# Optimization experiments

Hardware: AMD Instinct MI355X
Metric: run time of the kernel (lower is better)

## Reference

```python
import jax, jax.numpy as jnp
import numpy as np

EPS = 1e-5

def _conv3x3(x, w, b):
    # NCHW, OIHW, 3x3 stride 1 pad 1
    y = jax.lax.conv_general_dilated(x, w, window_strides=(1, 1),
                                     padding=((1, 1), (1, 1)),
                                     dimension_numbers=('NCHW', 'OIHW', 'NCHW'))
    return y + b[None, :, None, None]

def _pool_upsample(x, k):
    # adaptive avg pool to (H/k, W/k) then nearest block-upsample back
    B, C, H, W = x.shape
    p = x.reshape(B, C, H // k, k, W // k, k).mean(axis=(3, 5))
    return jnp.repeat(jnp.repeat(p, k, axis=2), k, axis=3)

def setup_inputs() -> dict:
    key = jax.random.key(0)
    ks = jax.random.split(key, 12)
    B, C, H, W = 32, 8, 300, 300
    d = {
        'x': jax.random.normal(ks[0], (B, C, H, W), jnp.float32),
        'w5': jax.random.normal(ks[1], (8, 16, 3, 3), jnp.float32) * 0.1,
        'b5': jnp.zeros((8,), jnp.float32),
        'w10': jax.random.normal(ks[2], (8, 16, 3, 3), jnp.float32) * 0.1,
        'b10': jnp.zeros((8,), jnp.float32),
        'w15': jax.random.normal(ks[3], (8, 16, 3, 3), jnp.float32) * 0.1,
        'b15': jnp.zeros((8,), jnp.float32),
        'gw': jax.random.normal(ks[4], (8, 24, 3, 3), jnp.float32) * 0.1,
        'gb': jnp.zeros((8,), jnp.float32),
        'mw': jax.random.normal(ks[5], (8, 24, 3, 3), jnp.float32) * 0.1,
        'mb': jnp.zeros((8,), jnp.float32),
        'gamma': jnp.ones((8,), jnp.float32),
        'beta': jnp.zeros((8,), jnp.float32),
    }
    return d

def reference(x, w5, b5, w10, b10, w15, b15, gw, gb, mw, mb, gamma, beta):
    up5 = _pool_upsample(x, 5)    # [B,8,300,300]
    up10 = _pool_upsample(x, 10)
    up15 = _pool_upsample(x, 15)
    c5 = _conv3x3(jnp.concatenate([x, up5], axis=1), w5, b5)
    c10 = _conv3x3(jnp.concatenate([x, up10], axis=1), w10, b10)
    c15 = _conv3x3(jnp.concatenate([x, up15], axis=1), w15, b15)
    g_in = jnp.concatenate([c5, c10, c15], axis=1)  # [B,24,H,W]
    # gated conv, activation=None: conv(g_in) * sigmoid(mask_conv(g_in))
    y = _conv3x3(g_in, gw, gb) * jax.nn.sigmoid(_conv3x3(g_in, mw, mb))
    # batch norm (training-mode batch stats, biased var, as torch default)
    mean = y.mean(axis=(0, 2, 3), keepdims=True)
    var = ((y - mean) ** 2).mean(axis=(0, 2, 3), keepdims=True)
    y = (y - mean) * jax.lax.rsqrt(var + EPS)
    return y * gamma[None, :, None, None] + beta[None, :, None, None]
```

## Files before the change

### kernel.cpp

```cpp
#include <hip/hip_runtime.h>
#include <math.h>

typedef __bf16 bfrag __attribute__((ext_vector_type(8)));
typedef __bf16 bf16x4 __attribute__((ext_vector_type(4)));
typedef __bf16 bf16x8 __attribute__((ext_vector_type(8)));
typedef float f32x4 __attribute__((ext_vector_type(4)));

#define BN 32
#define HH 300
#define WW 300
#define HW 90000
#define NPX (BN * HW)

#define GX 10
#define GY 19
#define CPX 612
#define XPX 720
#define CWSTRIDE 4896

#define P5I_BYTE_OFF   0
#define P10I_BYTE_OFF  1843200
#define P15I_BYTE_OFF  2304000
#define CWB_BYTE_OFF   2508800
#define GWB_BYTE_OFF   2524160
#define STAT_BYTE_OFF  2531328
#define SS_BYTE_OFF    2539520
#define XBF_BYTE_OFF   2539584
#define XBF_END        (XBF_BYTE_OFF + (size_t)NPX * 16)

__device__ __forceinline__ short f2bf(float f) {
    union { float f; unsigned u; } v;
    v.f = f;
    unsigned r = v.u + 0x7FFF + ((v.u >> 16) & 1);
    return (short)(r >> 16);
}

__device__ __forceinline__ float bf2f(unsigned short s) {
    union { unsigned u; float f; } v;
    v.u = ((unsigned)s) << 16;
    return v.f;
}

__device__ __forceinline__ void setup_body(int gid, int gstride,
                                           const float* __restrict__ w5,
                                           const float* __restrict__ w10,
                                           const float* __restrict__ w15,
                                           const float* __restrict__ gw,
                                           const float* __restrict__ mw,
                                           short* __restrict__ cBg,
                                           short* __restrict__ gBg,
                                           double* __restrict__ stats) {
    for (int idx = gid; idx < 7680; idx += gstride) {
        int s = idx / 2560, rem = idx % 2560;
        int n = rem / 160, r2 = rem % 160;
        int tap = r2 / 16, ci = r2 % 16;
        float v = 0.f;
        if (n < 8 && tap < 9) {
            const float* W = (s == 0) ? w5 : ((s == 1) ? w10 : w15);
            v = W[(n * 16 + ci) * 9 + tap];
        }
        cBg[idx] = f2bf(v);
    }
    for (int idx = gid; idx < 3584; idx += gstride) {
        int n = idx / 224, r2 = idx % 224;
        int blk = r2 / 8, cj = r2 % 8;
        float v = 0.f;
        if (blk < 27) {
            int tap = blk / 3, ci24 = (blk % 3) * 8 + cj;
            if (n < 8) v = gw[(n * 24 + ci24) * 9 + tap];
            else       v = mw[((n - 8) * 24 + ci24) * 9 + tap];
        }
        gBg[idx] = f2bf(v);
    }
    for (int idx = gid; idx < 16 * 64; idx += gstride) stats[idx] = 0.0;
}

__global__ void k_setup(const float* __restrict__ w5, const float* __restrict__ w10,
                        const float* __restrict__ w15, const float* __restrict__ gw,
                        const float* __restrict__ mw, short* __restrict__ cBg,
                        short* __restrict__ gBg, double* __restrict__ stats) {
    setup_body(threadIdx.x, 256, w5, w10, w15, gw, mw, cBg, gBg, stats);
}

__global__ __launch_bounds__(256) void k_xbf(const float* __restrict__ x,
                                             unsigned short* __restrict__ xbf,
                                             const float* __restrict__ w5,
                                             const float* __restrict__ w10,
                                             const float* __restrict__ w15,
                                             const float* __restrict__ gw,
                                             const float* __restrict__ mw,
                                             short* __restrict__ cBg,
                                             short* __restrict__ gBg,
                                             double* __restrict__ stats) {
    const int b = blockIdx.y;
    const int px = blockIdx.x * 256 + threadIdx.x;
    if (px < HW) {
        const float* xp = x + (size_t)b * 8 * HW + px;
        bf16x8 pk;
#pragma unroll
        for (int ch = 0; ch < 8; ch++) pk[ch] = (__bf16)xp[(size_t)ch * HW];
        *(bf16x8*)&xbf[((size_t)b * HW + px) * 8] = pk;
    }
    if (blockIdx.y == 0 && blockIdx.x < 16) {
        int gid = blockIdx.x * 256 + threadIdx.x;
        setup_body(gid, 4096, w5, w10, w15, gw, mw, cBg, gBg, stats);
    }
}

__global__ void k_pool5(const float* __restrict__ x, unsigned short* __restrict__ p5i) {
    int id = blockIdx.x * 256 + threadIdx.x;
    int bc = id / 3600, cell = id % 3600;
    int b = bc >> 3, c = bc & 7;
    int pi = cell / 60, pj = cell % 60;
    const float* rp = x + (size_t)bc * HW + pi * 5 * WW + pj * 5;
    float s = 0.f;
#pragma unroll
    for (int u = 0; u < 5; u++)
#pragma unroll
        for (int v = 0; v < 5; v++) s += rp[u * WW + v];
    p5i[((size_t)b * 3600 + cell) * 8 + c] = (unsigned short)f2bf(s * 0.04f);
}

__global__ __launch_bounds__(256) void k_pool5b(const unsigned short* __restrict__ xbf,
                                                unsigned short* __restrict__ p5i) {
    int id = blockIdx.x * 256 + threadIdx.x;
    int b = id / 3600, cell = id % 3600;
    int pi = cell / 60, pj = cell % 60;
    const unsigned short* base = xbf + ((size_t)b * HW + pi * 5 * WW + pj * 5) * 8;
    float s[8] = {0.f, 0.f, 0.f, 0.f, 0.f, 0.f, 0.f, 0.f};
#pragma unroll
    for (int u = 0; u < 5; u++)
#pragma unroll
        for (int v = 0; v < 5; v++) {
            bf16x8 vv = *(const bf16x8*)&base[(u * WW + v) * 8];
#pragma unroll
            for (int ch = 0; ch < 8; ch++) s[ch] += (float)vv[ch];
        }
    bf16x8 pk;
#pragma unroll
    for (int ch = 0; ch < 8; ch++) pk[ch] = (__bf16)(s[ch] * 0.04f);
    *(bf16x8*)&p5i[((size_t)b * 3600 + cell) * 8] = pk;
}

__global__ void k_poolD(const unsigned short* __restrict__ p5i,
                        unsigned short* __restrict__ p10i,
                        unsigned short* __restrict__ p15i) {
    int id = blockIdx.x * 256 + threadIdx.x;
    if (id < 230400) {
        int bc = id / 900, cell = id % 900;
        int b = bc >> 3, c = bc & 7;
        int pi = cell / 30, pj = cell % 30;
        const unsigned short* base = p5i + ((size_t)b * 3600) * 8 + c;
        float s = bf2f(base[((2 * pi) * 60 + 2 * pj) * 8]) +
                  bf2f(base[((2 * pi) * 60 + 2 * pj + 1) * 8]) +
                  bf2f(base[((2 * pi + 1) * 60 + 2 * pj) * 8]) +
                  bf2f(base[((2 * pi + 1) * 60 + 2 * pj + 1) * 8]);
        p10i[((size_t)b * 900 + cell) * 8 + c] = (unsigned short)f2bf(s * 0.25f);
    } else if (id < 332800) {
        int id2 = id - 230400;
        int bc = id2 / 400, cell = id2 % 400;
        int b = bc >> 3, c = bc & 7;
        int pi = cell / 20, pj = cell % 20;
        const unsigned short* base = p5i + ((size_t)b * 3600) * 8 + c;
        float s = 0.f;
#pragma unroll
        for (int u = 0; u < 3; u++)
#pragma unroll
            for (int v = 0; v < 3; v++)
                s += bf2f(base[((3 * pi + u) * 60 + 3 * pj + v) * 8]);
        p15i[((size_t)b * 400 + cell) * 8 + c] = (unsigned short)f2bf(s * (1.f / 9.f));
    }
}

template <int K, int PW>
__device__ __forceinline__ void up_load(const unsigned short* __restrict__ pooled,
                                        int b, int r0, int c0, int t, uint4* v) {
#pragma unroll
    for (int it = 0; it < 3; it++) {
        int idx = t + 256 * it;
        uint4 val = {0u, 0u, 0u, 0u};
        if (idx < XPX) {
            int i = idx / 36, j = idx - i * 36;
            int ra = r0 - 2 + i, ca = c0 - 2 + j;
            if (ra >= 0 && ra < HH && ca >= 0 && ca < WW) {
                int pi = (int)((unsigned)ra / K);
                int pj = (int)((unsigned)ca / K);
                val = *(const uint4*)&pooled[((size_t)b * (PW * PW) + pi * PW + pj) * 8];
            }
        }
        v[it] = val;
    }
}

__device__ __forceinline__ void up_store(short* xuU, int t, const uint4* v) {
#pragma unroll
    for (int it = 0; it < 3; it++) {
        int idx = t + 256 * it;
        if (idx < XPX) *(uint4*)&xuU[idx * 8] = v[it];
    }
}

__device__ __forceinline__ void c_phase(const short* xuX, const short* xuU,
                                        short* cwP,
                                        const unsigned short* __restrict__ cBs,
                                        const float* __restrict__ bias,
                                        int r0, int c0, int lane, int wid, bool edge) {
    const int n = lane & 15, quad = lane >> 4;
    const int qh = quad >> 1, ql = quad & 1;
    const short* xbase = ql ? xuU : xuX;
    bfrag wfr[5];
    int dpoff[5];
#pragma unroll
    for (int km = 0; km < 5; km++) {
        int tapw = km * 2 + qh;
        int tapa = (tapw > 8) ? 8 : tapw;
        wfr[km] = *(const bfrag*)&cBs[(n * 10 + tapw) * 16 + ql * 8];
        dpoff[km] = ((tapa / 3) * 36 + tapa % 3) * 8;
    }
    float bO[4];
#pragma unroll
    for (int r = 0; r < 4; r++) bO[r] = bias[(quad & 1) * 4 + r];

    for (int g = wid; g < 39; g += 4) {
        int px = g * 16 + n;
        if (px > 611) px = 611;
        int rp = (int)((unsigned)px / 34u);
        int cp = px - rp * 34;
        int pb = (rp * 36 + cp) * 8;
        f32x4 acc = {0.f, 0.f, 0.f, 0.f};
#pragma unroll
        for (int km = 0; km < 5; km++)
            acc = __builtin_amdgcn_mfma_f32_16x16x32_bf16(
                wfr[km], *(const bfrag*)&xbase[pb + dpoff[km]], acc, 0, 0, 0);
        if (quad < 2) {
            bf16x4 pk;
#pragma unroll
            for (int r = 0; r < 4; r++) pk[r] = (__bf16)(acc[r] + bO[r]);
            if (edge) {
                int ra = r0 - 1 + rp, ca = c0 - 1 + cp;
                if (ra < 0 || ra >= HH || ca < 0 || ca >= WW) {
#pragma unroll
                    for (int r = 0; r < 4; r++) pk[r] = (__bf16)0.f;
                }
            }
            *(bf16x4*)&cwP[px * 8 + quad * 4] = pk;
        }
    }
}

template <bool XBF>
__global__ __launch_bounds__(256, 3) void k_fused(
    const float* __restrict__ x, const unsigned short* __restrict__ xbf,
    const unsigned short* __restrict__ p5i, const unsigned short* __restrict__ p10i,
    const unsigned short* __restrict__ p15i,
    const unsigned short* __restrict__ cBg, const unsigned short* __restrict__ gBg,
    const float* __restrict__ b5, const float* __restrict__ b10, const float* __restrict__ b15,
    const float* __restrict__ gb, const float* __restrict__ mb,
    float* __restrict__ out, double* __restrict__ stats) {
    __shared__ __align__(16) short xuX[XPX * 8];
    __shared__ __align__(16) short xuU[XPX * 8];
    __shared__ __align__(16) short cwS[3 * CWSTRIDE];

    const int b = blockIdx.z;
    const int r0 = blockIdx.y * 16, c0 = blockIdx.x * 32;
    const int t = threadIdx.x, lane = t & 63, wid = t >> 6;
    const bool edge = (blockIdx.x == 0) | (blockIdx.x == GX - 1) |
                      (blockIdx.y == 0) | (blockIdx.y == GY - 1);

    uint4 upv[3];
    up_load<5, 60>(p5i, b, r0, c0, t, upv);

    if constexpr (XBF) {
#pragma unroll
        for (int it = 0; it < 3; it++) {
            int idx = t + 256 * it;
            if (idx < XPX) {
                int i = idx / 36, j = idx - i * 36;
                int ra = r0 - 2 + i, ca = c0 - 2 + j;
                uint4 v = {0u, 0u, 0u, 0u};
                if (ra >= 0 && ra < HH && ca >= 0 && ca < WW)
                    v = *(const uint4*)&xbf[((size_t)b * HW + ra * WW + ca) * 8];
                *(uint4*)&xuX[idx * 8] = v;
            }
        }
    } else {
        for (int idx = t; idx < 1440; idx += 256) {
            int cp = idx / 360, rem = idx % 360;
            int i = rem / 18, jp = rem % 18;
            int j = 2 * jp;
            int ra = r0 - 2 + i, ca = c0 - 2 + j;
            float2 v0 = {0.f, 0.f}, v1 = {0.f, 0.f};
            if (ra >= 0 && ra < HH && ca >= 0 && ca <= WW - 2) {
                size_t base = ((size_t)(b * 8 + 2 * cp) * HH + ra) * WW + ca;
                v0 = *(const float2*)&x[base];
                v1 = *(const float2*)&x[base + HW];
            }
            unsigned pA = (unsigned short)f2bf(v0.x) | ((unsigned)(unsigned short)f2bf(v1.x) << 16);
            unsigned pB = (unsigned short)f2bf(v0.y) | ((unsigned)(unsigned short)f2bf(v1.y) << 16);
            int px = i * 36 + j;
            *(unsigned*)&xuX[px * 8 + 2 * cp] = pA;
            *(unsigned*)&xuX[(px + 1) * 8 + 2 * cp] = pB;
        }
    }
    up_store(xuU, t, upv);
    __syncthreads();

    c_phase(xuX, xuU, cwS, cBg, b5, r0, c0, lane, wid, edge);
    up_load<10, 30>(p10i, b, r0, c0, t, upv);
    __syncthreads();
    up_store(xuU, t, upv);
    __syncthreads();

    c_phase(xuX, xuU, cwS + CWSTRIDE, cBg + 2560, b10, r0, c0, lane, wid, edge);
    up_load<15, 20>(p15i, b, r0, c0, t, upv);
    __syncthreads();
    up_store(xuU, t, upv);
    __syncthreads();

    c_phase(xuX, xuU, cwS + 2 * CWSTRIDE, cBg + 5120, b15, r0, c0, lane, wid, edge);
    __syncthreads();

    const int n = lane & 15, quad = lane >> 4;
    bfrag gfr[7];
    int goff[7];
#pragma unroll
    for (int km = 0; km < 7; km++) {
        int blkw = km * 4 + quad;
        int blka = (blkw > 26) ? 26 : blkw;
        gfr[km] = *(const bfrag*)&gBg[(n * 28 + blkw) * 8];
        int tap = blka / 3, cig = blka - tap * 3;
        goff[km] = cig * CWSTRIDE + ((tap / 3) * 34 + tap % 3) * 8;
    }
    float gO[4], mO[4];
#pragma unroll
    for (int r = 0; r < 4; r++) {
        gO[r] = gb[(quad & 1) * 4 + r];
        mO[r] = mb[(quad & 1) * 4 + r];
    }
    float ls[4] = {0.f, 0.f, 0.f, 0.f}, ls2[4] = {0.f, 0.f, 0.f, 0.f};

    for (int g = wid; g < 32; g += 4) {
        int px = g * 16 + n;
        int rr = px >> 5, cc = px & 31;
        int off0 = (rr * 34 + cc) * 8;
        f32x4 acc = {0.f, 0.f, 0.f, 0.f};
#pragma unroll
        for (int km = 0; km < 7; km++)
            acc = __builtin_amdgcn_mfma_f32_16x16x32_bf16(
                gfr[km], *(const bfrag*)&cwS[off0 + goff[km]], acc, 0, 0, 0);
        int ra = r0 + rr, ca = c0 + cc;
        bool wr = !edge || (ra < HH && ca < WW);
#pragma unroll
        for (int reg = 0; reg < 4; reg++) {
            float val;
            if (quad < 2) val = acc[reg] + gO[reg];
            else          val = __builtin_amdgcn_rcpf(1.f + __expf(-(acc[reg] + mO[reg])));
            float other = __shfl_xor(val, 32);
            if (quad < 2 && wr) {
                float y = val * other;
                int ch = quad * 4 + reg;
                out[(size_t)(b * 8 + ch) * HW + (size_t)ra * WW + ca] = y;
                ls[reg] += y;
                ls2[reg] += y * y;
            }
        }
    }
#pragma unroll
    for (int m = 1; m < 16; m <<= 1) {
#pragma unroll
        for (int r = 0; r < 4; r++) {
            ls[r] += __shfl_xor(ls[r], m);
            ls2[r] += __shfl_xor(ls2[r], m);
        }
    }
    if (n == 0 && quad < 2) {
        int hash = (blockIdx.x + GX * blockIdx.y + GX * GY * blockIdx.z) & 63;
#pragma unroll
        for (int r = 0; r < 4; r++) {
            atomicAdd(&stats[(quad * 4 + r) * 64 + hash], (double)ls[r]);
            atomicAdd(&stats[(8 + quad * 4 + r) * 64 + hash], (double)ls2[r]);
        }
    }
}

__global__ void k_stats(const double* __restrict__ stats, const float* __restrict__ gamma,
                        const float* __restrict__ beta, float* __restrict__ ss) {
    __shared__ double red[16][16];
    int t = threadIdx.x;
    int row = t >> 4, col = t & 15;
    double s = stats[row * 64 + col] + stats[row * 64 + col + 16] +
               stats[row * 64 + col + 32] + stats[row * 64 + col + 48];
    red[row][col] = s;
    __syncthreads();
    if (t < 16) {
        double tot = 0.0;
#pragma unroll
        for (int i = 0; i < 16; i++) tot += red[t][i];
        red[t][0] = tot;
    }
    __syncthreads();
    if (t < 8) {
        double N = (double)NPX;
        double mean = red[t][0] / N;
        double var = red[8 + t][0] / N - mean * mean;
        double scale = (double)gamma[t] / sqrt(var + 1e-5);
        ss[t] = (float)scale;
        ss[8 + t] = (float)((double)beta[t] - mean * scale);
    }
}

__global__ void k_norm(float* __restrict__ out, const float* __restrict__ ss) {
    int i = blockIdx.x * 256 + threadIdx.x;
    if (i < (BN * 8 * HW) / 4) {
        int plane = (i * 4) / HW;
        int ch = plane & 7;
        float sc = ss[ch], sh = ss[8 + ch];
        float4* p = (float4*)out + i;
        float4 v = *p;
        v.x = v.x * sc + sh;
        v.y = v.y * sc + sh;
        v.z = v.z * sc + sh;
        v.w = v.w * sc + sh;
        *p = v;
    }
}

extern "C" void kernel_launch(void* const* d_in, const int* in_sizes, int n_in,
                              void* d_out, int out_size, void* d_ws, size_t ws_size,
                              hipStream_t stream) {
    const float* x = (const float*)d_in[0];
    const float* w5 = (const float*)d_in[1];
    const float* b5 = (const float*)d_in[2];
    const float* w10 = (const float*)d_in[3];
    const float* b10 = (const float*)d_in[4];
    const float* w15 = (const float*)d_in[5];
    const float* b15 = (const float*)d_in[6];
    const float* gw = (const float*)d_in[7];
    const float* gb = (const float*)d_in[8];
    const float* mw = (const float*)d_in[9];
    const float* mb = (const float*)d_in[10];
    const float* gamma = (const float*)d_in[11];
    const float* beta = (const float*)d_in[12];

    float* out = (float*)d_out;
    unsigned short* p5i = (unsigned short*)((char*)d_ws + P5I_BYTE_OFF);
    unsigned short* p10i = (unsigned short*)((char*)d_ws + P10I_BYTE_OFF);
    unsigned short* p15i = (unsigned short*)((char*)d_ws + P15I_BYTE_OFF);
    short* cBg = (short*)((char*)d_ws + CWB_BYTE_OFF);
    short* gBg = (short*)((char*)d_ws + GWB_BYTE_OFF);
    double* stats = (double*)((char*)d_ws + STAT_BYTE_OFF);
    float* ss = (float*)((char*)d_ws + SS_BYTE_OFF);
    unsigned short* xbf = (unsigned short*)((char*)d_ws + XBF_BYTE_OFF);

    const bool use_xbf = (ws_size >= XBF_END);

    dim3 grid(GX, GY, BN);
    if (use_xbf) {
        k_xbf<<<dim3(352, 32), 256, 0, stream>>>(x, xbf, w5, w10, w15, gw, mw,
                                                 cBg, gBg, stats);
        k_pool5b<<<450, 256, 0, stream>>>(xbf, p5i);
        k_poolD<<<1300, 256, 0, stream>>>(p5i, p10i, p15i);
        k_fused<true><<<grid, 256, 0, stream>>>(x, xbf, p5i, p10i, p15i,
                                                (const unsigned short*)cBg, (const unsigned short*)gBg,
                                                b5, b10, b15, gb, mb, out, stats);
    } else {
        k_setup<<<1, 256, 0, stream>>>(w5, w10, w15, gw, mw, cBg, gBg, stats);
        k_pool5<<<3600, 256, 0, stream>>>(x, p5i);
        k_poolD<<<1300, 256, 0, stream>>>(p5i, p10i, p15i);
        k_fused<false><<<grid, 256, 0, stream>>>(x, xbf, p5i, p10i, p15i,
                                                 (const unsigned short*)cBg, (const unsigned short*)gBg,
                                                 b5, b10, b15, gb, mb, out, stats);
    }
    k_stats<<<1, 256, 0, stream>>>(stats, gamma, beta, ss);
    k_norm<<<(BN * 8 * HW / 4 + 255) / 256, 256, 0, stream>>>(out, ss);
}
```

Before: 387.4 us.

## Use padded per-batch bf16 slabs and fuse pooling into one prep kernel

Adds a new path that writes x plus the 5/10/15 pooled maps into zero-padded per-batch bf16 slabs in a single prep kernel, with pool10 and pool15 derived from pool5 in shared memory. The fused conv kernel then gathers MFMA operands straight from global memory through row/column offset lookup tables, with no staging of inputs into LDS, and padding removes the bounds checks. This cuts the number of launches and the separate pooling passes. It needs a larger workspace, and it relies on uncoalesced global gathers hitting in cache.

```diff
diff --git a/kernel.cpp b/kernel.cpp
--- a/kernel.cpp
+++ b/kernel.cpp
@@ -27,6 +27,21 @@
 #define SS_BYTE_OFF    2539520
 #define XBF_BYTE_OFF   2539584
 #define XBF_END        (XBF_BYTE_OFF + (size_t)NPX * 16)
+
+#define XW 302
+#define P5W 62
+#define P10W 32
+#define P15W 22
+#define XOFF5  (XW * XW * 16)
+#define XOFF10 (XOFF5 + P5W * P5W * 16)
+#define XOFF15 (XOFF10 + P10W * P10W * 16)
+#define SLAB   (XOFF15 + P15W * P15W * 16)
+#define CWB2_OFF  0
+#define GWB2_OFF  15360
+#define STAT2_OFF 22528
+#define SS2_OFF   30720
+#define SLAB_OFF  32768
+#define NEW_END   (SLAB_OFF + (size_t)BN * SLAB)
 
 __device__ __forceinline__ short f2bf(float f) {
     union { float f; unsigned u; } v;
@@ -80,6 +95,266 @@
                         const float* __restrict__ mw, short* __restrict__ cBg,
                         short* __restrict__ gBg, double* __restrict__ stats) {
     setup_body(threadIdx.x, 256, w5, w10, w15, gw, mw, cBg, gBg, stats);
+}
+
+__global__ __launch_bounds__(256) void k_prep2(const float* __restrict__ x,
+                                               char* __restrict__ slabs,
+                                               const float* __restrict__ w5,
+                                               const float* __restrict__ w10,
+                                               const float* __restrict__ w15,
+                                               const float* __restrict__ gw,
+                                               const float* __restrict__ mw,
+                                               short* __restrict__ cBg,
+                                               short* __restrict__ gBg,
+                                               double* __restrict__ stats) {
+    __shared__ __align__(16) short p5L[3600 * 8];
+    const int b = blockIdx.y, t = threadIdx.x;
+    char* slab = slabs + (size_t)b * SLAB;
+
+    if (blockIdx.x < 357) {
+        int p = blockIdx.x * 256 + t;
+        if (p < XW * XW) {
+            int pr = p / XW, pc = p - pr * XW;
+            if (pr >= 1 && pr <= 300 && pc >= 1 && pc <= 300) {
+                const float* xp = x + (size_t)b * 8 * HW + (pr - 1) * WW + (pc - 1);
+                bf16x8 pk;
+#pragma unroll
+                for (int ch = 0; ch < 8; ch++) pk[ch] = (__bf16)xp[ch * HW];
+                *(bf16x8*)(slab + (size_t)p * 16) = pk;
+            } else {
+                uint4 z = {0u, 0u, 0u, 0u};
+                *(uint4*)(slab + (size_t)p * 16) = z;
+            }
+        }
+        if (blockIdx.y == 0 && blockIdx.x < 16)
+            setup_body(blockIdx.x * 256 + t, 4096, w5, w10, w15, gw, mw, cBg, gBg, stats);
+        return;
+    }
+
+    const float* xb = x + (size_t)b * 8 * HW;
+    for (int cell = t; cell < 3600; cell += 256) {
+        int pi = cell / 60, pj = cell - pi * 60;
+        const float* rp0 = xb + (pi * 5) * WW + pj * 5;
+        float s[8] = {0.f, 0.f, 0.f, 0.f, 0.f, 0.f, 0.f, 0.f};
+#pragma unroll
+        for (int ch = 0; ch < 8; ch++)
+#pragma unroll
+            for (int u = 0; u < 5; u++)
+#pragma unroll
+                for (int v = 0; v < 5; v++) s[ch] += rp0[ch * HW + u * WW + v];
+        bf16x8 pk;
+#pragma unroll
+        for (int ch = 0; ch < 8; ch++) pk[ch] = (__bf16)(s[ch] * 0.04f);
+        *(bf16x8*)&p5L[cell * 8] = pk;
+        *(bf16x8*)(slab + XOFF5 + ((size_t)(pi + 1) * P5W + (pj + 1)) * 16) = pk;
+    }
+    uint4 z = {0u, 0u, 0u, 0u};
+    for (int i = t; i < P5W * P5W; i += 256) {
+        int r = i / P5W, c = i - r * P5W;
+        if (r == 0 || r == P5W - 1 || c == 0 || c == P5W - 1)
+            *(uint4*)(slab + XOFF5 + (size_t)i * 16) = z;
+    }
+    for (int i = t; i < P10W * P10W; i += 256) {
+        int r = i / P10W, c = i - r * P10W;
+        if (r == 0 || r == P10W - 1 || c == 0 || c == P10W - 1)
+            *(uint4*)(slab + XOFF10 + (size_t)i * 16) = z;
+    }
+    for (int i = t; i < P15W * P15W; i += 256) {
+        int r = i / P15W, c = i - r * P15W;
+        if (r == 0 || r == P15W - 1 || c == 0 || c == P15W - 1)
+            *(uint4*)(slab + XOFF15 + (size_t)i * 16) = z;
+    }
+    __syncthreads();
+    for (int cell = t; cell < 900; cell += 256) {
+        int pi = cell / 30, pj = cell - pi * 30;
+        bf16x8 a = *(bf16x8*)&p5L[((2 * pi) * 60 + 2 * pj) * 8];
+        bf16x8 bb = *(bf16x8*)&p5L[((2 * pi) * 60 + 2 * pj + 1) * 8];
+        bf16x8 c = *(bf16x8*)&p5L[((2 * pi + 1) * 60 + 2 * pj) * 8];
+        bf16x8 d = *(bf16x8*)&p5L[((2 * pi + 1) * 60 + 2 * pj + 1) * 8];
+        bf16x8 pk;
+#pragma unroll
+        for (int ch = 0; ch < 8; ch++)
+            pk[ch] = (__bf16)(((float)a[ch] + (float)bb[ch] + (float)c[ch] + (float)d[ch]) * 0.25f);
+        *(bf16x8*)(slab + XOFF10 + ((size_t)(pi + 1) * P10W + (pj + 1)) * 16) = pk;
+    }
+    for (int cell = t; cell < 400; cell += 256) {
+        int pi = cell / 20, pj = cell - pi * 20;
+        float s[8] = {0.f, 0.f, 0.f, 0.f, 0.f, 0.f, 0.f, 0.f};
+#pragma unroll
+        for (int u = 0; u < 3; u++)
+#pragma unroll
+            for (int v = 0; v < 3; v++) {
+                bf16x8 vv = *(bf16x8*)&p5L[((3 * pi + u) * 60 + 3 * pj + v) * 8];
+#pragma unroll
+                for (int ch = 0; ch < 8; ch++) s[ch] += (float)vv[ch];
+            }
+        bf16x8 pk;
+#pragma unroll
+        for (int ch = 0; ch < 8; ch++) pk[ch] = (__bf16)(s[ch] * (1.f / 9.f));
+        *(bf16x8*)(slab + XOFF15 + ((size_t)(pi + 1) * P15W + (pj + 1)) * 16) = pk;
+    }
+}
+
+__device__ __forceinline__ void c_phase2(const char* __restrict__ sb, short* cwP,
+                                         const unsigned short* __restrict__ cBs,
+                                         const float* __restrict__ bias, int lset,
+                                         const int lutR[4][20], const int lutC[4][36],
+                                         int r0, int c0, int lane, int wid, bool edge) {
+    const int n = lane & 15, quad = lane >> 4;
+    const int qh = quad >> 1, ql = quad & 1;
+    bfrag wfr[5];
+    int diA[5], djA[5];
+#pragma unroll
+    for (int km = 0; km < 5; km++) {
+        int tapw = km * 2 + qh;
+        int tapa = (tapw > 8) ? 8 : tapw;
+        wfr[km] = *(const bfrag*)&cBs[(n * 10 + tapw) * 16 + ql * 8];
+        diA[km] = tapa / 3;
+        djA[km] = tapa - diA[km] * 3;
+    }
+    const int* lr = lutR[ql ? lset : 0];
+    const int* lc = lutC[ql ? lset : 0];
+    float bO[4];
+#pragma unroll
+    for (int r = 0; r < 4; r++) bO[r] = bias[(quad & 1) * 4 + r];
+
+#pragma unroll 2
+    for (int g = wid; g < 39; g += 4) {
+        int px = g * 16 + n;
+        if (px > 611) px = 611;
+        int rp = (int)((unsigned)px / 34u);
+        int cp = px - rp * 34;
+        f32x4 acc = {0.f, 0.f, 0.f, 0.f};
+#pragma unroll
+        for (int km = 0; km < 5; km++) {
+            int off = lr[rp + diA[km]] + lc[cp + djA[km]];
+            acc = __builtin_amdgcn_mfma_f32_16x16x32_bf16(
+                wfr[km], *(const bfrag*)(sb + off), acc, 0, 0, 0);
+        }
+        if (quad < 2) {
+            bf16x4 pk;
+#pragma unroll
+            for (int r = 0; r < 4; r++) pk[r] = (__bf16)(acc[r] + bO[r]);
+            if (edge) {
+                int ra = r0 - 1 + rp, ca = c0 - 1 + cp;
+                if (ra < 0 || ra >= HH || ca < 0 || ca >= WW) {
+#pragma unroll
+                    for (int r = 0; r < 4; r++) pk[r] = (__bf16)0.f;
+                }
+            }
+            *(bf16x4*)&cwP[px * 8 + quad * 4] = pk;
+        }
+    }
+}
+
+__global__ __launch_bounds__(256, 5) void k_fused2(
+    const char* __restrict__ slabs,
+    const unsigned short* __restrict__ cBg, const unsigned short* __restrict__ gBg,
+    const float* __restrict__ b5, const float* __restrict__ b10, const float* __restrict__ b15,
+    const float* __restrict__ gb, const float* __restrict__ mb,
+    float* __restrict__ out, double* __restrict__ stats) {
+    __shared__ __align__(16) short cwS[3 * CWSTRIDE];
+    __shared__ int lutR[4][20];
+    __shared__ int lutC[4][36];
+
+    const int b = blockIdx.z;
+    const int r0 = blockIdx.y * 16, c0 = blockIdx.x * 32;
+    const int t = threadIdx.x, lane = t & 63, wid = t >> 6;
+    const bool edge = (blockIdx.x == 0) | (blockIdx.x == GX - 1) |
+                      (blockIdx.y == 0) | (blockIdx.y == GY - 1);
+
+    if (t < 224) {
+        int set = t / 56, e = t % 56;
+        if (e < 20) {
+            int r = r0 - 2 + e;
+            r = (r < -1) ? -1 : ((r > 300) ? 300 : r);
+            int v;
+            if (set == 0)      v = (r + 1) * (XW * 16);
+            else if (set == 1) v = XOFF5 + (int)(((unsigned)(r + 5) / 5u) * (P5W * 16));
+            else if (set == 2) v = XOFF10 + (int)(((unsigned)(r + 10) / 10u) * (P10W * 16));
+            else               v = XOFF15 + (int)(((unsigned)(r + 15) / 15u) * (P15W * 16));
+            lutR[set][e] = v;
+        } else {
+            int j = e - 20;
+            int c = c0 - 2 + j;
+            c = (c < -1) ? -1 : ((c > 300) ? 300 : c);
+            int v;
+            if (set == 0)      v = (c + 1) * 16;
+            else if (set == 1) v = (int)(((unsigned)(c + 5) / 5u) * 16);
+            else if (set == 2) v = (int)(((unsigned)(c + 10) / 10u) * 16);
+            else               v = (int)(((unsigned)(c + 15) / 15u) * 16);
+            lutC[set][j] = v;
+        }
+    }
+    __syncthreads();
+
+    const char* sb = slabs + (size_t)b * SLAB;
+    c_phase2(sb, cwS,                cBg,        b5,  1, lutR, lutC, r0, c0, lane, wid, edge);
+    c_phase2(sb, cwS + CWSTRIDE,     cBg + 2560, b10, 2, lutR, lutC, r0, c0, lane, wid, edge);
+    c_phase2(sb, cwS + 2 * CWSTRIDE, cBg + 5120, b15, 3, lutR, lutC, r0, c0, lane, wid, edge);
+    __syncthreads();
+
+    const int n = lane & 15, quad = lane >> 4;
+    bfrag gfr[7];
+    int goff[7];
+#pragma unroll
+    for (int km = 0; km < 7; km++) {
+        int blkw = km * 4 + quad;
+        int blka = (blkw > 26) ? 26 : blkw;
+        gfr[km] = *(const bfrag*)&gBg[(n * 28 + blkw) * 8];
+        int tap = blka / 3, cig = blka - tap * 3;
+        goff[km] = cig * CWSTRIDE + ((tap / 3) * 34 + tap % 3) * 8;
+    }
+    float gO[4], mO[4];
+#pragma unroll
+    for (int r = 0; r < 4; r++) {
+        gO[r] = gb[(quad & 1) * 4 + r];
+        mO[r] = mb[(quad & 1) * 4 + r];
+    }
+    float ls[4] = {0.f, 0.f, 0.f, 0.f}, ls2[4] = {0.f, 0.f, 0.f, 0.f};
+
+    for (int g = wid; g < 32; g += 4) {
+        int px = g * 16 + n;
+        int rr = px >> 5, cc = px & 31;
+        int off0 = (rr * 34 + cc) * 8;
+        f32x4 acc = {0.f, 0.f, 0.f, 0.f};
+#pragma unroll
+        for (int km = 0; km < 7; km++)
+            acc = __builtin_amdgcn_mfma_f32_16x16x32_bf16(
+                gfr[km], *(const bfrag*)&cwS[off0 + goff[km]], acc, 0, 0, 0);
+        int ra = r0 + rr, ca = c0 + cc;
+        bool wr = !edge || (ra < HH && ca < WW);
+#pragma unroll
+        for (int reg = 0; reg < 4; reg++) {
+            float val;
+            if (quad < 2) val = acc[reg] + gO[reg];
+            else          val = __builtin_amdgcn_rcpf(1.f + __expf(-(acc[reg] + mO[reg])));
+            float other = __shfl_xor(val, 32);
+            if (quad < 2 && wr) {
+                float y = val * other;
+                int ch = quad * 4 + reg;
+                out[(size_t)(b * 8 + ch) * HW + (size_t)ra * WW + ca] = y;
+                ls[reg] += y;
+                ls2[reg] += y * y;
+            }
+        }
+    }
+#pragma unroll
+    for (int m = 1; m < 16; m <<= 1) {
+#pragma unroll
+        for (int r = 0; r < 4; r++) {
+            ls[r] += __shfl_xor(ls[r], m);
+            ls2[r] += __shfl_xor(ls2[r], m);
+        }
+    }
+    if (n == 0 && quad < 2) {
+        int hash = (blockIdx.x + GX * blockIdx.y + GX * GY * blockIdx.z) & 63;
+#pragma unroll
+        for (int r = 0; r < 4; r++) {
+            atomicAdd(&stats[(quad * 4 + r) * 64 + hash], (double)ls[r]);
+            atomicAdd(&stats[(8 + quad * 4 + r) * 64 + hash], (double)ls2[r]);
+        }
+    }
 }
 
 __global__ __launch_bounds__(256) void k_xbf(const float* __restrict__ x,
@@ -441,8 +716,25 @@
     const float* mb = (const float*)d_in[10];
     const float* gamma = (const float*)d_in[11];
     const float* beta = (const float*)d_in[12];
-
     float* out = (float*)d_out;
+
+    if (ws_size >= NEW_END) {
+        short* cBg = (short*)((char*)d_ws + CWB2_OFF);
+        short* gBg = (short*)((char*)d_ws + GWB2_OFF);
+        double* stats = (double*)((char*)d_ws + STAT2_OFF);
+        float* ss = (float*)((char*)d_ws + SS2_OFF);
+        char* slabs = (char*)d_ws + SLAB_OFF;
+
+        k_prep2<<<dim3(358, BN), 256, 0, stream>>>(x, slabs, w5, w10, w15, gw, mw,
+                                                   cBg, gBg, stats);
+        k_fused2<<<dim3(GX, GY, BN), 256, 0, stream>>>(
+            slabs, (const unsigned short*)cBg, (const unsigned short*)gBg,
+            b5, b10, b15, gb, mb, out, stats);
+        k_stats<<<1, 256, 0, stream>>>(stats, gamma, beta, ss);
+        k_norm<<<(BN * 8 * HW / 4 + 255) / 256, 256, 0, stream>>>(out, ss);
+        return;
+    }
+
     unsigned short* p5i = (unsigned short*)((char*)d_ws + P5I_BYTE_OFF);
     unsigned short* p10i = (unsigned short*)((char*)d_ws + P10I_BYTE_OFF);
     unsigned short* p15i = (unsigned short*)((char*)d_ws + P15I_BYTE_OFF);
@@ -453,7 +745,6 @@
     unsigned short* xbf = (unsigned short*)((char*)d_ws + XBF_BYTE_OFF);
 
     const bool use_xbf = (ws_size >= XBF_END);
-
     dim3 grid(GX, GY, BN);
     if (use_xbf) {
         k_xbf<<<dim3(352, 32), 256, 0, stream>>>(x, xbf, w5, w10, w15, gw, mw,
```

New measurement: 477.6 us. 1.23x slower.

## Add fused kernel reading compact pooled tiles and accumulating gated conv per branch

Applied to the files above, without the earlier changes.

Adds a new fused kernel that loads only the small pooled-grid tiles into LDS rather than materialising upsampled pooled values, and computes the upsample index on the fly for each tap. It runs the three branch convolutions one at a time into two alternating LDS buffers and adds each branch's share to the gated/mask convolution accumulators straight away. This needs far less LDS, which allows a higher occupancy hint (launch bounds 256,5). It also adds a per-branch weight layout for the gate convolution. The path is used only when the workspace is large enough to hold the extra weight buffer.

```diff
diff --git a/kernel.cpp b/kernel.cpp
--- a/kernel.cpp
+++ b/kernel.cpp
@@ -27,6 +27,16 @@
 #define SS_BYTE_OFF    2539520
 #define XBF_BYTE_OFF   2539584
 #define XBF_END        (XBF_BYTE_OFF + (size_t)NPX * 16)
+#define GW3_BYTE_OFF   XBF_END
+#define NEW3_END       (GW3_BYTE_OFF + 9216)
+
+#define XU3_OFF   0
+#define P5_OFF3   11520
+#define P10_OFF3  12160
+#define P15_OFF3  12400
+#define CW0_OFF3  12592
+#define CW1_OFF3  22384
+#define LDS3_SIZE 32176
 
 __device__ __forceinline__ short f2bf(float f) {
     union { float f; unsigned u; } v;
@@ -49,6 +59,7 @@
                                            const float* __restrict__ mw,
                                            short* __restrict__ cBg,
                                            short* __restrict__ gBg,
+                                           short* __restrict__ gB3,
                                            double* __restrict__ stats) {
     for (int idx = gid; idx < 7680; idx += gstride) {
         int s = idx / 2560, rem = idx % 2560;
@@ -72,6 +83,20 @@
         }
         gBg[idx] = f2bf(v);
     }
+    if (gB3) {
+        for (int idx = gid; idx < 4608; idx += gstride) {
+            int s = idx / 1536, rem = idx % 1536;
+            int n = rem / 96, r2 = rem % 96;
+            int slot = r2 / 8, cj = r2 % 8;
+            float v = 0.f;
+            if (slot < 9) {
+                int ci24 = s * 8 + cj;
+                if (n < 8) v = gw[(n * 24 + ci24) * 9 + slot];
+                else       v = mw[((n - 8) * 24 + ci24) * 9 + slot];
+            }
+            gB3[idx] = f2bf(v);
+        }
+    }
     for (int idx = gid; idx < 16 * 64; idx += gstride) stats[idx] = 0.0;
 }
 
@@ -79,7 +104,7 @@
                         const float* __restrict__ w15, const float* __restrict__ gw,
                         const float* __restrict__ mw, short* __restrict__ cBg,
                         short* __restrict__ gBg, double* __restrict__ stats) {
-    setup_body(threadIdx.x, 256, w5, w10, w15, gw, mw, cBg, gBg, stats);
+    setup_body(threadIdx.x, 256, w5, w10, w15, gw, mw, cBg, gBg, nullptr, stats);
 }
 
 __global__ __launch_bounds__(256) void k_xbf(const float* __restrict__ x,
@@ -91,6 +116,7 @@
                                              const float* __restrict__ mw,
                                              short* __restrict__ cBg,
                                              short* __restrict__ gBg,
+                                             short* __restrict__ gB3,
                                              double* __restrict__ stats) {
     const int b = blockIdx.y;
     const int px = blockIdx.x * 256 + threadIdx.x;
@@ -103,22 +129,8 @@
     }
     if (blockIdx.y == 0 && blockIdx.x < 16) {
         int gid = blockIdx.x * 256 + threadIdx.x;
-        setup_body(gid, 4096, w5, w10, w15, gw, mw, cBg, gBg, stats);
-    }
-}
-
-__global__ void k_pool5(const float* __restrict__ x, unsigned short* __restrict__ p5i) {
-    int id = blockIdx.x * 256 + threadIdx.x;
-    int bc = id / 3600, cell = id % 3600;
-    int b = bc >> 3, c = bc & 7;
-    int pi = cell / 60, pj = cell % 60;
-    const float* rp = x + (size_t)bc * HW + pi * 5 * WW + pj * 5;
-    float s = 0.f;
-#pragma unroll
-    for (int u = 0; u < 5; u++)
-#pragma unroll
-        for (int v = 0; v < 5; v++) s += rp[u * WW + v];
-    p5i[((size_t)b * 3600 + cell) * 8 + c] = (unsigned short)f2bf(s * 0.04f);
+        setup_body(gid, 4096, w5, w10, w15, gw, mw, cBg, gBg, gB3, stats);
+    }
 }
 
 __global__ __launch_bounds__(256) void k_pool5b(const unsigned short* __restrict__ xbf,
@@ -172,6 +184,234 @@
     }
 }
 
+template <int K, int PCOLS>
+__device__ __forceinline__ void c_phase3(char* LDSp, int cwOff, int patchOff,
+                                         const unsigned short* __restrict__ cBs,
+                                         const float* __restrict__ bias,
+                                         int pr0, int pc0,
+                                         int r0, int c0, int lane, int wid, bool edge) {
+    constexpr int T0[5] = {0, 2, 4, 6, 8};
+    constexpr int T1[5] = {1, 3, 5, 7, 8};
+    const int n = lane & 15, quad = lane >> 4;
+    const int qh = quad >> 1, ql = quad & 1;
+    bfrag wfr[5];
+#pragma unroll
+    for (int km = 0; km < 5; km++) {
+        int tapw = km * 2 + qh;
+        wfr[km] = *(const bfrag*)&cBs[(n * 10 + tapw) * 16 + ql * 8];
+    }
+    const int srow = patchOff - pr0 * (PCOLS * 16);
+    const int scol = -(pc0 << 4);
+    float bO[4];
+#pragma unroll
+    for (int r = 0; r < 4; r++) bO[r] = bias[(quad & 1) * 4 + r];
+
+    for (int g = wid; g < 39; g += 4) {
+        int px = g * 16 + n;
+        if (px > 611) px = 611;
+        int rp = (int)((unsigned)px / 34u);
+        int cp = px - rp * 34;
+        int xb = (rp * 36 + cp) * 16;
+        int rowB[3], colB[3];
+#pragma unroll
+        for (int d = 0; d < 3; d++) {
+            rowB[d] = (int)(((unsigned)(r0 - 2 + rp + d + K) / (unsigned)K) * (PCOLS * 16)) + srow;
+            colB[d] = (int)(((unsigned)(c0 - 2 + cp + d + K) / (unsigned)K) << 4) + scol;
+        }
+        f32x4 acc = {0.f, 0.f, 0.f, 0.f};
+#pragma unroll
+        for (int km = 0; km < 5; km++) {
+            int au0 = rowB[T0[km] / 3] + colB[T0[km] % 3];
+            int au1 = rowB[T1[km] / 3] + colB[T1[km] % 3];
+            int ax0 = xb + ((T0[km] / 3) * 36 + (T0[km] % 3)) * 16;
+            int ax1 = xb + ((T1[km] / 3) * 36 + (T1[km] % 3)) * 16;
+            int au = qh ? au1 : au0;
+            int ax = qh ? ax1 : ax0;
+            int ad = ql ? au : ax;
+            acc = __builtin_amdgcn_mfma_f32_16x16x32_bf16(
+                wfr[km], *(const bfrag*)(LDSp + ad), acc, 0, 0, 0);
+        }
+        if (quad < 2) {
+            bf16x4 pk;
+#pragma unroll
+            for (int r = 0; r < 4; r++) pk[r] = (__bf16)(acc[r] + bO[r]);
+            if (edge) {
+                int ra = r0 - 1 + rp, ca = c0 - 1 + cp;
+                if (ra < 0 || ra >= HH || ca < 0 || ca >= WW) {
+#pragma unroll
+                    for (int r = 0; r < 4; r++) pk[r] = (__bf16)0.f;
+                }
+            }
+            *(bf16x4*)(LDSp + cwOff + px * 16 + quad * 8) = pk;
+        }
+    }
+}
+
+__device__ __forceinline__ void gate_partial(const char* LDSp, int cwOff,
+                                             const unsigned short* __restrict__ gB3s,
+                                             int lane, int wid, f32x4* acc) {
+    const int n = lane & 15, quad = lane >> 4;
+    bfrag gfr[3];
+    int goffB[3];
+#pragma unroll
+    for (int km = 0; km < 3; km++) {
+        int slot = km * 4 + quad;
+        int tap = (slot > 8) ? 8 : slot;
+        gfr[km] = *(const bfrag*)&gB3s[(n * 12 + slot) * 8];
+        int di = tap / 3, dj = tap - di * 3;
+        goffB[km] = (di * 34 + dj) * 16;
+    }
+#pragma unroll
+    for (int gi = 0; gi < 8; gi++) {
+        int g = wid + 4 * gi;
+        int px = g * 16 + n;
+        int off0 = cwOff + ((px >> 5) * 34 + (px & 31)) * 16;
+#pragma unroll
+        for (int km = 0; km < 3; km++)
+            acc[gi] = __builtin_amdgcn_mfma_f32_16x16x32_bf16(
+                gfr[km], *(const bfrag*)(LDSp + off0 + goffB[km]), acc[gi], 0, 0, 0);
+    }
+}
+
+__global__ __launch_bounds__(256, 5) void k_fused3(
+    const unsigned short* __restrict__ xbf,
+    const unsigned short* __restrict__ p5i, const unsigned short* __restrict__ p10i,
+    const unsigned short* __restrict__ p15i,
+    const unsigned short* __restrict__ cBg, const unsigned short* __restrict__ gB3,
+    const float* __restrict__ b5, const float* __restrict__ b10, const float* __restrict__ b15,
+    const float* __restrict__ gb, const float* __restrict__ mb,
+    float* __restrict__ out, double* __restrict__ stats) {
+    __shared__ __align__(16) char LDS[LDS3_SIZE];
+
+    const int b = blockIdx.z;
+    const int r0 = blockIdx.y * 16, c0 = blockIdx.x * 32;
+    const int t = threadIdx.x, lane = t & 63, wid = t >> 6;
+    const bool edge = (blockIdx.x == 0) | (blockIdx.x == GX - 1) |
+                      (blockIdx.y == 0) | (blockIdx.y == GY - 1);
+
+    const int pr0_5 = (r0 + 3) / 5, pc0_5 = (c0 + 3) / 5;
+    const int pr0_10 = (r0 + 8) / 10, pc0_10 = (c0 + 8) / 10;
+    const int pr0_15 = (r0 + 13) / 15, pc0_15 = (c0 + 13) / 15;
+
+#pragma unroll
+    for (int it = 0; it < 3; it++) {
+        int idx = t + 256 * it;
+        if (idx < XPX) {
+            int i = idx / 36, j = idx - i * 36;
+            int ra = r0 - 2 + i, ca = c0 - 2 + j;
+            uint4 v = {0u, 0u, 0u, 0u};
+            if (ra >= 0 && ra < HH && ca >= 0 && ca < WW)
+                v = *(const uint4*)&xbf[((size_t)b * HW + ra * WW + ca) * 8];
+            *(uint4*)(LDS + XU3_OFF + idx * 16) = v;
+        }
+    }
+    if (t < 67) {
+        const unsigned short* src;
+        int off;
+        bool valid;
+        if (t < 40) {
+            int a = t >> 3, cc = t & 7;
+            int ci = pr0_5 - 1 + a, cj = pc0_5 - 1 + cc;
+            valid = (ci >= 0) && (ci < 60) && (cj >= 0) && (cj < 60);
+            src = p5i + ((size_t)b * 3600 + ci * 60 + cj) * 8;
+            off = P5_OFF3 + t * 16;
+        } else if (t < 55) {
+            int i2 = t - 40;
+            int a = i2 / 5, cc = i2 % 5;
+            int ci = pr0_10 - 1 + a, cj = pc0_10 - 1 + cc;
+            valid = (ci >= 0) && (ci < 30) && (cj >= 0) && (cj < 30);
+            src = p10i + ((size_t)b * 900 + ci * 30 + cj) * 8;
+            off = P10_OFF3 + i2 * 16;
+        } else {
+            int i2 = t - 55;
+            int a = i2 >> 2, cc = i2 & 3;
+            int ci = pr0_15 - 1 + a, cj = pc0_15 - 1 + cc;
+            valid = (ci >= 0) && (ci < 20) && (cj >= 0) && (cj < 20);
+            src = p15i + ((size_t)b * 400 + ci * 20 + cj) * 8;
+            off = P15_OFF3 + i2 * 16;
+        }
+        uint4 v = {0u, 0u, 0u, 0u};
+        if (valid) v = *(const uint4*)src;
+        *(uint4*)(LDS + off) = v;
+    }
+    __syncthreads();
+
+    f32x4 acc[8];
+#pragma unroll
+    for (int gi = 0; gi < 8; gi++) acc[gi] = (f32x4){0.f, 0.f, 0.f, 0.f};
+
+    c_phase3<5, 8>(LDS, CW0_OFF3, P5_OFF3, cBg, b5, pr0_5, pc0_5, r0, c0, lane, wid, edge);
+    __syncthreads();
+    gate_partial(LDS, CW0_OFF3, gB3, lane, wid, acc);
+    c_phase3<10, 5>(LDS, CW1_OFF3, P10_OFF3, cBg + 2560, b10, pr0_10, pc0_10, r0, c0, lane, wid, edge);
+    __syncthreads();
+    gate_partial(LDS, CW1_OFF3, gB3 + 1536, lane, wid, acc);
+    c_phase3<15, 4>(LDS, CW0_OFF3, P15_OFF3, cBg + 5120, b15, pr0_15, pc0_15, r0, c0, lane, wid, edge);
+    __syncthreads();
+    gate_partial(LDS, CW0_OFF3, gB3 + 3072, lane, wid, acc);
+
+    const int n = lane & 15, quad = lane >> 4;
+    float gO[4], mO[4];
+#pragma unroll
+    for (int r = 0; r < 4; r++) {
+        gO[r] = gb[(quad & 1) * 4 + r];
+        mO[r] = mb[(quad & 1) * 4 + r];
+    }
+    float ls[4] = {0.f, 0.f, 0.f, 0.f}, ls2[4] = {0.f, 0.f, 0.f, 0.f};
+#pragma unroll
+    for (int gi = 0; gi < 8; gi++) {
+        int g = wid + 4 * gi;
+        int px = g * 16 + n;
+        int rr = px >> 5, cc = px & 31;
+        int ra = r0 + rr, ca = c0 + cc;
+        bool wr = !edge || (ra < HH && ca < WW);
+#pragma unroll
+        for (int reg = 0; reg < 4; reg++) {
+            float val;
+            if (quad < 2) val = acc[gi][reg] + gO[reg];
+            else          val = __builtin_amdgcn_rcpf(1.f + __expf(-(acc[gi][reg] + mO[reg])));
+            float other = __shfl_xor(val, 32);
+            if (quad < 2 && wr) {
+                float y = val * other;
+                int ch = quad * 4 + reg;
+                out[(size_t)(b * 8 + ch) * HW + (size_t)ra * WW + ca] = y;
+                ls[reg] += y;
+                ls2[reg] += y * y;
+            }
+        }
+    }
+#pragma unroll
+    for (int m = 1; m < 16; m <<= 1) {
+#pragma unroll
+        for (int r = 0; r < 4; r++) {
+            ls[r] += __shfl_xor(ls[r], m);
+            ls2[r] += __shfl_xor(ls2[r], m);
+        }
+    }
+    if (n == 0 && quad < 2) {
+        int hash = (blockIdx.x + GX * blockIdx.y + GX * GY * blockIdx.z) & 63;
+#pragma unroll
+        for (int r = 0; r < 4; r++) {
+            atomicAdd(&stats[(quad * 4 + r) * 64 + hash], (double)ls[r]);
+            atomicAdd(&stats[(8 + quad * 4 + r) * 64 + hash], (double)ls2[r]);
+        }
+    }
+}
+
+__global__ void k_pool5(const float* __restrict__ x, unsigned short* __restrict__ p5i) {
+    int id = blockIdx.x * 256 + threadIdx.x;
+    int bc = id / 3600, cell = id % 3600;
+    int b = bc >> 3, c = bc & 7;
+    int pi = cell / 60, pj = cell % 60;
+    const float* rp = x + (size_t)bc * HW + pi * 5 * WW + pj * 5;
+    float s = 0.f;
+#pragma unroll
+    for (int u = 0; u < 5; u++)
+#pragma unroll
+        for (int v = 0; v < 5; v++) s += rp[u * WW + v];
+    p5i[((size_t)b * 3600 + cell) * 8 + c] = (unsigned short)f2bf(s * 0.04f);
+}
+
 template <int K, int PW>
 __device__ __forceinline__ void up_load(const unsigned short* __restrict__ pooled,
                                         int b, int r0, int c0, int t, uint4* v) {
@@ -441,8 +681,8 @@
     const float* mb = (const float*)d_in[10];
     const float* gamma = (const float*)d_in[11];
     const float* beta = (const float*)d_in[12];
-
     float* out = (float*)d_out;
+
     unsigned short* p5i = (unsigned short*)((char*)d_ws + P5I_BYTE_OFF);
     unsigned short* p10i = (unsigned short*)((char*)d_ws + P10I_BYTE_OFF);
     unsigned short* p15i = (unsigned short*)((char*)d_ws + P15I_BYTE_OFF);
@@ -451,13 +691,20 @@
     double* stats = (double*)((char*)d_ws + STAT_BYTE_OFF);
     float* ss = (float*)((char*)d_ws + SS_BYTE_OFF);
     unsigned short* xbf = (unsigned short*)((char*)d_ws + XBF_BYTE_OFF);
-
-    const bool use_xbf = (ws_size >= XBF_END);
+    short* gB3 = (short*)((char*)d_ws + GW3_BYTE_OFF);
 
     dim3 grid(GX, GY, BN);
-    if (use_xbf) {
+    if (ws_size >= NEW3_END) {
         k_xbf<<<dim3(352, 32), 256, 0, stream>>>(x, xbf, w5, w10, w15, gw, mw,
-                                                 cBg, gBg, stats);
+                                                 cBg, gBg, gB3, stats);
+        k_pool5b<<<450, 256, 0, stream>>>(xbf, p5i);
+        k_poolD<<<1300, 256, 0, stream>>>(p5i, p10i, p15i);
+        k_fused3<<<grid, 256, 0, stream>>>(xbf, p5i, p10i, p15i,
+                                           (const unsigned short*)cBg, (const unsigned short*)gB3,
+                                           b5, b10, b15, gb, mb, out, stats);
+    } else if (ws_size >= XBF_END) {
+        k_xbf<<<dim3(352, 32), 256, 0, stream>>>(x, xbf, w5, w10, w15, gw, mw,
+                                                 cBg, gBg, nullptr, stats);
         k_pool5b<<<450, 256, 0, stream>>>(xbf, p5i);
         k_poolD<<<1300, 256, 0, stream>>>(p5i, p10i, p15i);
         k_fused<true><<<grid, 256, 0, stream>>>(x, xbf, p5i, p10i, p15i,
```

New measurement: 424.6 us. +9.6%, slower.
